# Kernel tuning notes

Hardware: AMD Instinct MI355X
Metric: run time of the kernel (lower is better)

## Reference

```python
import jax, jax.numpy as jnp
import numpy as np

B, N, F_IN = 8, 1024, 25   # batch, num_edges (GAT nodes), features_per_link = 1 + 8*num_bands
H, D = 8, 16               # num_heads, output_dim per head (hidden_size // num_heads)
NEG_INF = -9e15            # matches torch -9000000000000000.0


def setup_inputs() -> dict:
    key = jax.random.key(0)
    k1, k2, k3, k4 = jax.random.split(key, 4)
    node_feats = jax.random.normal(k1, (B, N, F_IN), dtype=jnp.float32)
    adj = jax.random.randint(k2, (B, N, N), 0, 2, dtype=jnp.int32)
    # Xavier-uniform-ish params per GATLayer.reset_parameters (gain for relu)
    gain = float(np.sqrt(2.0))
    limW = gain * np.sqrt(6.0 / (F_IN + D))
    lima = gain * np.sqrt(6.0 / (2 * D + 1))
    W = jax.random.uniform(k3, (H, F_IN, D), jnp.float32, -limW, limW)
    a = jax.random.uniform(k4, (H, 2 * D, 1), jnp.float32, -lima, lima)
    return {"node_feats": node_feats, "adj": adj, "W": W, "a": a}


def reference(node_feats, adj, W, a):
    d = W.shape[-1]
    # Wh: [B, H, N, D]
    Wh = jnp.einsum('bnf,hfd->bhnd', node_feats, W)
    # Additive attention: e_ij = <Wh_i, a_src> + <Wh_j, a_dst>  (no LeakyReLU in this module)
    a_src = a[:, :d, 0]   # [H, D]
    a_dst = a[:, d:, 0]   # [H, D]
    ei = jnp.einsum('bhnd,hd->bhn', Wh, a_src)  # [B, H, N]
    ej = jnp.einsum('bhnd,hd->bhn', Wh, a_dst)  # [B, H, N]
    e = ei[:, :, :, None] + ej[:, :, None, :]   # [B, H, N, N]
    mask = adj[:, None, :, :].astype(bool)      # [B, 1->H, N, N]
    e = jnp.where(mask, e, jnp.asarray(NEG_INF, e.dtype))
    alpha = jax.nn.softmax(e, axis=-1)          # dropout is identity at eval
    h_prime = jnp.einsum('bhij,bhjd->bhid', alpha, Wh)        # [B, H, N, D]
    h_prime = h_prime.transpose(0, 2, 1, 3).reshape(node_feats.shape[0], node_feats.shape[1], -1)
    return jax.nn.relu(h_prime), alpha
```

## Files before the change

### kernel.cpp

```cpp
#include <hip/hip_runtime.h>

#define L2E 1.44269504f

typedef short short8_t  __attribute__((ext_vector_type(8)));
typedef float fltx4     __attribute__((ext_vector_type(4)));
typedef int   intx4     __attribute__((ext_vector_type(4)));
typedef unsigned short ushort4_t __attribute__((ext_vector_type(4)));
typedef unsigned int uint32;

__device__ __forceinline__ unsigned short f2bf(float f) {
    uint32 u = __float_as_uint(f);
    u += 0x7FFFu + ((u >> 16) & 1u);
    return (unsigned short)(u >> 16);
}

__global__ __launch_bounds__(256) void prep_once(
    const float* __restrict__ x,
    const float* __restrict__ W,
    const float* __restrict__ a,
    float* __restrict__ pexp_ws,
    unsigned short* __restrict__ whb)
{
    int t  = blockIdx.x * 256 + threadIdx.x;
    int bh = t >> 10, n = t & 1023;
    int b  = bh >> 3, h = bh & 7;

    const float* xr = x + ((size_t)(b * 1024 + n)) * 25;
    const float* Wp = W + h * 400;
    const float* ap = a + h * 32;

    float xf[25];
    #pragma unroll
    for (int f = 0; f < 25; ++f) xf[f] = xr[f];

    int base = ((bh * 32 + (n >> 5)) * 64 + ((n >> 3) & 3) * 16) * 8 + (n & 7);
    float vj = 0.f;
    #pragma unroll
    for (int d = 0; d < 16; ++d) {
        float s = 0.f;
        #pragma unroll
        for (int f = 0; f < 25; ++f) s += xf[f] * Wp[f * 16 + d];
        vj += s * ap[16 + d];
        whb[base + d * 8] = f2bf(s);
    }
    pexp_ws[t] = exp2f(vj * L2E);
}

__global__ __launch_bounds__(256) void gat_main(
    const int*   __restrict__ adj,
    const float* __restrict__ pexp_ws,
    const unsigned short* __restrict__ whb,
    float* __restrict__ out0,
    float* __restrict__ out1)
{
    __shared__ __align__(16) unsigned short palds[16 * 1024];

    const int blk   = blockIdx.x;
    const int x8    = blk & 7;
    const int h     = (blk >> 3) & 7;
    const int s     = blk >> 6;
    const int c     = s * 8 + x8;
    const int b     = c >> 6;
    const int chunk = c & 63;
    const int bh    = b * 8 + h;
    const int wave  = threadIdx.x >> 6;
    const int lane  = threadIdx.x & 63;
    const int i0    = chunk * 16;

    const fltx4* pe4 = (const fltx4*)(pexp_ws + bh * 1024);
    fltx4 expr_[4];
    #pragma unroll
    for (int j0 = 0; j0 < 4; ++j0) expr_[j0] = pe4[j0 * 64 + lane];

    float* abase = out1 + (size_t)bh * 1024 * 1024;
    char*  ldsb  = (char*)palds;

    const intx4* adjb = (const intx4*)(adj + ((size_t)b * 1024 + i0 + wave * 4) * 1024);
    uint32 msk[4];
    #pragma unroll
    for (int r = 0; r < 4; ++r) {
        uint32 m = 0;
        #pragma unroll
        for (int j0 = 0; j0 < 4; ++j0) {
            intx4 a4 = adjb[r * 256 + j0 * 64 + lane];
            m |= (a4.x ? (1u << (j0 * 4 + 0)) : 0u);
            m |= (a4.y ? (1u << (j0 * 4 + 1)) : 0u);
            m |= (a4.z ? (1u << (j0 * 4 + 2)) : 0u);
            m |= (a4.w ? (1u << (j0 * 4 + 3)) : 0u);
        }
        msk[r] = m;
    }

    float sum[4];
    #pragma unroll
    for (int r = 0; r < 4; ++r) {
        float s0 = 0.f;
        const uint32 m = msk[r];
        #pragma unroll
        for (int j0 = 0; j0 < 4; ++j0) {
            fltx4 ev = expr_[j0];
            s0 += ((m >> (j0 * 4 + 0)) & 1u) ? ev.x : 0.f;
            s0 += ((m >> (j0 * 4 + 1)) & 1u) ? ev.y : 0.f;
            s0 += ((m >> (j0 * 4 + 2)) & 1u) ? ev.z : 0.f;
            s0 += ((m >> (j0 * 4 + 3)) & 1u) ? ev.w : 0.f;
        }
        sum[r] = s0;
    }

    #pragma unroll
    for (int off = 32; off; off >>= 1) {
        #pragma unroll
        for (int r = 0; r < 4; ++r) sum[r] += __shfl_xor(sum[r], off);
    }

    #pragma unroll
    for (int r = 0; r < 4; ++r) {
        const int rl = wave * 4 + r;
        const int i  = i0 + rl;
        const uint32 m = msk[r];
        const bool ok = sum[r] > 0.f;
        const float rinv = ok ? __builtin_amdgcn_rcpf(sum[r]) : 0.f;
        const float fb   = ok ? 0.f : (1.0f / 1024.0f);

        float* arow = abase + (size_t)i * 1024;
        const int swz  = (rl & 7) << 4;
        char* lrow = ldsb + rl * 2048;
        #pragma unroll
        for (int j0 = 0; j0 < 4; ++j0) {
            fltx4 ev = expr_[j0];
            fltx4 st;
            st.x = ((m >> (j0 * 4 + 0)) & 1u) ? ev.x * rinv + fb : fb;
            st.y = ((m >> (j0 * 4 + 1)) & 1u) ? ev.y * rinv + fb : fb;
            st.z = ((m >> (j0 * 4 + 2)) & 1u) ? ev.z * rinv + fb : fb;
            st.w = ((m >> (j0 * 4 + 3)) & 1u) ? ev.w * rinv + fb : fb;
            *(fltx4*)(arow + (j0 * 64 + lane) * 4) = st;
            ushort4_t bv;
            bv.x = f2bf(st.x); bv.y = f2bf(st.y);
            bv.z = f2bf(st.z); bv.w = f2bf(st.w);
            *(ushort4_t*)(lrow + (((j0 * 512) + lane * 8) ^ swz)) = bv;
        }
    }

    __syncthreads();

    if (wave == 0) {
        const int mrow = lane & 15;
        const int quad = lane >> 4;
        const int swz  = (mrow & 7) << 4;
        char* lrow = ldsb + mrow * 2048;
        const unsigned short* bbase = whb + (size_t)bh * 16384;

        fltx4 acc = {0.f, 0.f, 0.f, 0.f};
        #pragma unroll 4
        for (int ks = 0; ks < 32; ++ks) {
            short8_t afr = *(const short8_t*)(lrow + ((ks * 64 + quad * 16) ^ swz));
            short8_t bfr = *(const short8_t*)(bbase + ((ks * 64 + lane) << 3));
            acc = __builtin_amdgcn_mfma_f32_16x16x32_bf16(afr, bfr, acc, 0, 0, 0);
        }

        #pragma unroll
        for (int r = 0; r < 4; ++r) {
            int i = i0 + quad * 4 + r;
            float v = acc[r] > 0.f ? acc[r] : 0.f;
            out0[((size_t)(b * 1024 + i)) * 128 + h * 16 + mrow] = v;
        }
    }
}

__global__ __launch_bounds__(256) void gat_fused(
    const float* __restrict__ x, const int* __restrict__ adj,
    const float* __restrict__ W, const float* __restrict__ a,
    float* __restrict__ out0, float* __restrict__ out1)
{
    __shared__ __align__(16) unsigned short whb[32 * 64 * 8];
    __shared__ __align__(16) float ej_lds[1024];
    __shared__ float ei_lds[64];
    __shared__ float wa[64];

    const int bh    = blockIdx.x >> 4;
    const int chunk = blockIdx.x & 15;
    const int b     = bh >> 3;
    const int h     = bh & 7;
    const int tid   = threadIdx.x;
    const int wave  = tid >> 6;
    const int lane  = tid & 63;
    const int mrow  = lane & 15;
    const int quad  = lane >> 4;

    const float* Wp = W + h * 400;
    const float* ap = a + h * 32;
    const float* xb = x + (size_t)b * 1024 * 25;

    if (tid < 50) {
        int f = tid % 25, which = tid / 25;
        float s = 0.f;
        #pragma unroll
        for (int d = 0; d < 16; ++d) s += Wp[f * 16 + d] * ap[which * 16 + d];
        wa[which * 32 + f] = s;
    }
    __syncthreads();

    for (int s = 0; s < 4; ++s) {
        int n = tid + (s << 8);
        const float* xr = xb + n * 25;
        float xf[25];
        #pragma unroll
        for (int f = 0; f < 25; ++f) xf[f] = xr[f];
        float vi = 0.f, vj = 0.f;
        #pragma unroll
        for (int f = 0; f < 25; ++f) { vi += xf[f] * wa[f]; vj += xf[f] * wa[32 + f]; }
        ej_lds[n] = vj;
        if ((n >> 6) == chunk) ei_lds[n & 63] = vi;
        int base = (((n >> 5) * 64 + ((n >> 3) & 3) * 16) << 3) + (n & 7);
        #pragma unroll
        for (int d = 0; d < 16; ++d) {
            float s2 = 0.f;
            #pragma unroll
            for (int f = 0; f < 25; ++f) s2 += xf[f] * Wp[f * 16 + d];
            whb[base + d * 8] = f2bf(s2);
        }
    }
    __syncthreads();

    const int i0 = chunk * 64 + wave * 16;
    float* abase = out1 + (size_t)bh * 1024 * 1024;
    const fltx4* ej4 = (const fltx4*)ej_lds;

    for (int r = 0; r < 16; ++r) {
        int i = i0 + r;
        float s_ei = ei_lds[wave * 16 + r];
        const intx4* adj4 = (const intx4*)(adj + ((size_t)b * 1024 + i) * 1024);
        float p[16];
        float sum = 0.f;
        #pragma unroll
        for (int j0 = 0; j0 < 4; ++j0) {
            intx4 av = adj4[j0 * 64 + lane];
            fltx4 ev = ej4[j0 * 64 + lane];
            float p0 = av.x ? exp2f((s_ei + ev.x) * L2E) : 0.f;
            float p1 = av.y ? exp2f((s_ei + ev.y) * L2E) : 0.f;
            float p2 = av.z ? exp2f((s_ei + ev.z) * L2E) : 0.f;
            float p3 = av.w ? exp2f((s_ei + ev.w) * L2E) : 0.f;
            p[j0 * 4 + 0] = p0; p[j0 * 4 + 1] = p1;
            p[j0 * 4 + 2] = p2; p[j0 * 4 + 3] = p3;
            sum += (p0 + p1) + (p2 + p3);
        }
        #pragma unroll
        for (int off = 32; off; off >>= 1) sum += __shfl_xor(sum, off);
        float rinv;
        if (sum > 0.f) {
            rinv = __builtin_amdgcn_rcpf(sum);
        } else {
            rinv = 1.0f;
            #pragma unroll
            for (int k = 0; k < 16; ++k) p[k] = 1.0f / 1024.0f;
        }
        float* arow = abase + (size_t)i * 1024;
        #pragma unroll
        for (int j0 = 0; j0 < 4; ++j0) {
            fltx4 st;
            st.x = p[j0 * 4 + 0] * rinv; st.y = p[j0 * 4 + 1] * rinv;
            st.z = p[j0 * 4 + 2] * rinv; st.w = p[j0 * 4 + 3] * rinv;
            *(fltx4*)(arow + (j0 * 64 + lane) * 4) = st;
        }
    }

    __builtin_amdgcn_fence(__ATOMIC_ACQ_REL, "workgroup");

    const float* aptr = abase + (size_t)(i0 + mrow) * 1024 + quad * 8;
    fltx4 acc = {0.f, 0.f, 0.f, 0.f};
    for (int ks = 0; ks < 32; ++ks) {
        fltx4 a0 = *(const fltx4*)(aptr + ks * 32);
        fltx4 a1 = *(const fltx4*)(aptr + ks * 32 + 4);
        short8_t afr;
        #pragma unroll
        for (int q = 0; q < 4; ++q) {
            afr[q]     = (short)f2bf(a0[q]);
            afr[4 + q] = (short)f2bf(a1[q]);
        }
        short8_t bfr = *(const short8_t*)&whb[((ks * 64 + lane) << 3)];
        acc = __builtin_amdgcn_mfma_f32_16x16x32_bf16(afr, bfr, acc, 0, 0, 0);
    }
    #pragma unroll
    for (int r = 0; r < 4; ++r) {
        int i = i0 + quad * 4 + r;
        float v = acc[r] > 0.f ? acc[r] : 0.f;
        out0[((size_t)(b * 1024 + i)) * 128 + h * 16 + mrow] = v;
    }
}

extern "C" void kernel_launch(void* const* d_in, const int* in_sizes, int n_in,
                              void* d_out, int out_size, void* d_ws, size_t ws_size,
                              hipStream_t stream) {
    const float* x   = (const float*)d_in[0];
    const int*   adj = (const int*)d_in[1];
    const float* W   = (const float*)d_in[2];
    const float* a   = (const float*)d_in[3];

    float* out0 = (float*)d_out;
    float* out1 = out0 + (size_t)8 * 1024 * 128;

    const size_t WHB_BYTES = (size_t)64 * 16384 * 2;
    const size_t EJ_BYTES  = (size_t)64 * 1024 * 4;
    const size_t NEED      = WHB_BYTES + EJ_BYTES;

    if (ws_size >= NEED) {
        unsigned short* whb = (unsigned short*)d_ws;
        float* pexp_ws = (float*)((char*)d_ws + WHB_BYTES);
        prep_once<<<256, 256, 0, stream>>>(x, W, a, pexp_ws, whb);
        gat_main<<<4096, 256, 0, stream>>>(adj, pexp_ws, whb, out0, out1);
    } else {
        gat_fused<<<1024, 256, 0, stream>>>(x, adj, W, a, out0, out1);
    }
}
```

Before: 330.4 us.

## Give each wave its own 16-row tile with per-wave MFMA, drop block barrier

Each wave now handles 16 query rows instead of 4, so every wave runs its own bf16 MFMA accumulation from a private LDS tile. The block-wide __syncthreads and the wave-0-only matmul go away, and the grid shrinks from 4096 to 1024 blocks. Alpha rows are written with nontemporal stores, interleaved column block by column block with the MFMA k-steps. This removes the idle waves during the matmul and the barrier stall. In exchange each thread holds 16 mask and sum registers, which may lower occupancy, and there is less block-level parallelism.

```diff
diff --git a/kernel.cpp b/kernel.cpp
--- a/kernel.cpp
+++ b/kernel.cpp
@@ -53,19 +53,19 @@
     float* __restrict__ out0,
     float* __restrict__ out1)
 {
-    __shared__ __align__(16) unsigned short palds[16 * 1024];
+    __shared__ __align__(16) unsigned short tlds[4][16][256];
 
     const int blk   = blockIdx.x;
     const int x8    = blk & 7;
     const int h     = (blk >> 3) & 7;
     const int s     = blk >> 6;
     const int c     = s * 8 + x8;
-    const int b     = c >> 6;
-    const int chunk = c & 63;
+    const int b     = c >> 4;
+    const int chunk = c & 15;
     const int bh    = b * 8 + h;
     const int wave  = threadIdx.x >> 6;
     const int lane  = threadIdx.x & 63;
-    const int i0    = chunk * 16;
+    const int i0    = chunk * 64 + wave * 16;
 
     const fltx4* pe4 = (const fltx4*)(pexp_ws + bh * 1024);
     fltx4 expr_[4];
@@ -73,12 +73,11 @@
     for (int j0 = 0; j0 < 4; ++j0) expr_[j0] = pe4[j0 * 64 + lane];
 
     float* abase = out1 + (size_t)bh * 1024 * 1024;
-    char*  ldsb  = (char*)palds;
-
-    const intx4* adjb = (const intx4*)(adj + ((size_t)b * 1024 + i0 + wave * 4) * 1024);
-    uint32 msk[4];
-    #pragma unroll
-    for (int r = 0; r < 4; ++r) {
+
+    const intx4* adjb = (const intx4*)(adj + ((size_t)b * 1024 + i0) * 1024);
+    uint32 msk[16];
+    #pragma unroll
+    for (int r = 0; r < 16; ++r) {
         uint32 m = 0;
         #pragma unroll
         for (int j0 = 0; j0 < 4; ++j0) {
@@ -91,9 +90,9 @@
         msk[r] = m;
     }
 
-    float sum[4];
-    #pragma unroll
-    for (int r = 0; r < 4; ++r) {
+    float sum[16];
+    #pragma unroll
+    for (int r = 0; r < 16; ++r) {
         float s0 = 0.f;
         const uint32 m = msk[r];
         #pragma unroll
@@ -106,64 +105,53 @@
         }
         sum[r] = s0;
     }
-
     #pragma unroll
     for (int off = 32; off; off >>= 1) {
         #pragma unroll
-        for (int r = 0; r < 4; ++r) sum[r] += __shfl_xor(sum[r], off);
-    }
-
-    #pragma unroll
-    for (int r = 0; r < 4; ++r) {
-        const int rl = wave * 4 + r;
-        const int i  = i0 + rl;
-        const uint32 m = msk[r];
-        const bool ok = sum[r] > 0.f;
-        const float rinv = ok ? __builtin_amdgcn_rcpf(sum[r]) : 0.f;
-        const float fb   = ok ? 0.f : (1.0f / 1024.0f);
-
-        float* arow = abase + (size_t)i * 1024;
-        const int swz  = (rl & 7) << 4;
-        char* lrow = ldsb + rl * 2048;
-        #pragma unroll
-        for (int j0 = 0; j0 < 4; ++j0) {
-            fltx4 ev = expr_[j0];
+        for (int r = 0; r < 16; ++r) sum[r] += __shfl_xor(sum[r], off);
+    }
+
+    char* tl = (char*)&tlds[wave][0][0];
+    const unsigned short* bbase = whb + (size_t)bh * 16384;
+    const int mrow = lane & 15;
+    const int quad = lane >> 4;
+    fltx4 acc = {0.f, 0.f, 0.f, 0.f};
+
+    #pragma unroll
+    for (int j0 = 0; j0 < 4; ++j0) {
+        fltx4 ev = expr_[j0];
+        #pragma unroll
+        for (int r = 0; r < 16; ++r) {
+            const bool ok = sum[r] > 0.f;
+            const float rinv = ok ? __builtin_amdgcn_rcpf(sum[r]) : 0.f;
+            const float fbv  = ok ? 0.f : (1.0f / 1024.0f);
+            const uint32 m = msk[r] >> (j0 * 4);
             fltx4 st;
-            st.x = ((m >> (j0 * 4 + 0)) & 1u) ? ev.x * rinv + fb : fb;
-            st.y = ((m >> (j0 * 4 + 1)) & 1u) ? ev.y * rinv + fb : fb;
-            st.z = ((m >> (j0 * 4 + 2)) & 1u) ? ev.z * rinv + fb : fb;
-            st.w = ((m >> (j0 * 4 + 3)) & 1u) ? ev.w * rinv + fb : fb;
-            *(fltx4*)(arow + (j0 * 64 + lane) * 4) = st;
+            st.x = (m & 1u) ? ev.x * rinv + fbv : fbv;
+            st.y = (m & 2u) ? ev.y * rinv + fbv : fbv;
+            st.z = (m & 4u) ? ev.z * rinv + fbv : fbv;
+            st.w = (m & 8u) ? ev.w * rinv + fbv : fbv;
+            __builtin_nontemporal_store(st,
+                (fltx4*)(abase + (size_t)(i0 + r) * 1024 + j0 * 256 + lane * 4));
             ushort4_t bv;
             bv.x = f2bf(st.x); bv.y = f2bf(st.y);
             bv.z = f2bf(st.z); bv.w = f2bf(st.w);
-            *(ushort4_t*)(lrow + (((j0 * 512) + lane * 8) ^ swz)) = bv;
-        }
-    }
-
-    __syncthreads();
-
-    if (wave == 0) {
-        const int mrow = lane & 15;
-        const int quad = lane >> 4;
-        const int swz  = (mrow & 7) << 4;
-        char* lrow = ldsb + mrow * 2048;
-        const unsigned short* bbase = whb + (size_t)bh * 16384;
-
-        fltx4 acc = {0.f, 0.f, 0.f, 0.f};
-        #pragma unroll 4
-        for (int ks = 0; ks < 32; ++ks) {
-            short8_t afr = *(const short8_t*)(lrow + ((ks * 64 + quad * 16) ^ swz));
-            short8_t bfr = *(const short8_t*)(bbase + ((ks * 64 + lane) << 3));
+            *(ushort4_t*)(tl + r * 512 + ((lane * 8) ^ ((r & 7) << 4))) = bv;
+        }
+        #pragma unroll
+        for (int kl = 0; kl < 8; ++kl) {
+            short8_t afr = *(const short8_t*)(tl + mrow * 512 +
+                             ((kl * 64 + quad * 16) ^ ((mrow & 7) << 4)));
+            short8_t bfr = *(const short8_t*)(bbase + (((j0 * 8 + kl) * 64 + lane) << 3));
             acc = __builtin_amdgcn_mfma_f32_16x16x32_bf16(afr, bfr, acc, 0, 0, 0);
         }
-
-        #pragma unroll
-        for (int r = 0; r < 4; ++r) {
-            int i = i0 + quad * 4 + r;
-            float v = acc[r] > 0.f ? acc[r] : 0.f;
-            out0[((size_t)(b * 1024 + i)) * 128 + h * 16 + mrow] = v;
-        }
+    }
+
+    #pragma unroll
+    for (int r = 0; r < 4; ++r) {
+        const int i = i0 + quad * 4 + r;
+        float v = acc[r] > 0.f ? acc[r] : 0.f;
+        out0[((size_t)(b * 1024 + i)) * 128 + h * 16 + mrow] = v;
     }
 }
 
@@ -307,7 +295,7 @@
         unsigned short* whb = (unsigned short*)d_ws;
         float* pexp_ws = (float*)((char*)d_ws + WHB_BYTES);
         prep_once<<<256, 256, 0, stream>>>(x, W, a, pexp_ws, whb);
-        gat_main<<<4096, 256, 0, stream>>>(adj, pexp_ws, whb, out0, out1);
+        gat_main<<<1024, 256, 0, stream>>>(adj, pexp_ws, whb, out0, out1);
     } else {
         gat_fused<<<1024, 256, 0, stream>>>(x, adj, W, a, out0, out1);
     }
```

After: 366.7 us. 1.11x slower.

## Loop heads inside each block to reuse adjacency mask and give every wave MFMA work

Applied to the files above, without the earlier changes.

Each block now handles all 8 heads for a 16-row chunk, so the adjacency mask is loaded and packed once instead of once per head, and the grid shrinks from 4096 to 512 blocks. Each wave writes its own 4 rows into a private LDS tile and runs its own MFMA with only rows 0-3 meaningful, which removes the block-wide barrier and the single-wave GEMM tail. The alpha output now uses nontemporal stores. The cost is that three quarters of each MFMA's rows are wasted, and there are fewer, longer-running blocks to hide memory latency.

```diff
diff --git a/kernel.cpp b/kernel.cpp
--- a/kernel.cpp
+++ b/kernel.cpp
@@ -53,29 +53,18 @@
     float* __restrict__ out0,
     float* __restrict__ out1)
 {
-    __shared__ __align__(16) unsigned short palds[16 * 1024];
+    __shared__ __align__(16) unsigned short tlds[4][4][1024];
 
     const int blk   = blockIdx.x;
-    const int x8    = blk & 7;
-    const int h     = (blk >> 3) & 7;
-    const int s     = blk >> 6;
-    const int c     = s * 8 + x8;
-    const int b     = c >> 6;
-    const int chunk = c & 63;
-    const int bh    = b * 8 + h;
+    const int b     = blk >> 6;
+    const int chunk = blk & 63;
     const int wave  = threadIdx.x >> 6;
     const int lane  = threadIdx.x & 63;
-    const int i0    = chunk * 16;
-
-    const fltx4* pe4 = (const fltx4*)(pexp_ws + bh * 1024);
-    fltx4 expr_[4];
-    #pragma unroll
-    for (int j0 = 0; j0 < 4; ++j0) expr_[j0] = pe4[j0 * 64 + lane];
-
-    float* abase = out1 + (size_t)bh * 1024 * 1024;
-    char*  ldsb  = (char*)palds;
-
-    const intx4* adjb = (const intx4*)(adj + ((size_t)b * 1024 + i0 + wave * 4) * 1024);
+    const int i0    = chunk * 16 + wave * 4;
+    const int mrow  = lane & 15;
+    const int quad  = lane >> 4;
+
+    const intx4* adjb = (const intx4*)(adj + ((size_t)b * 1024 + i0) * 1024);
     uint32 msk[4];
     #pragma unroll
     for (int r = 0; r < 4; ++r) {
@@ -91,78 +80,77 @@
         msk[r] = m;
     }
 
-    float sum[4];
-    #pragma unroll
-    for (int r = 0; r < 4; ++r) {
-        float s0 = 0.f;
-        const uint32 m = msk[r];
-        #pragma unroll
-        for (int j0 = 0; j0 < 4; ++j0) {
-            fltx4 ev = expr_[j0];
-            s0 += ((m >> (j0 * 4 + 0)) & 1u) ? ev.x : 0.f;
-            s0 += ((m >> (j0 * 4 + 1)) & 1u) ? ev.y : 0.f;
-            s0 += ((m >> (j0 * 4 + 2)) & 1u) ? ev.z : 0.f;
-            s0 += ((m >> (j0 * 4 + 3)) & 1u) ? ev.w : 0.f;
-        }
-        sum[r] = s0;
-    }
-
-    #pragma unroll
-    for (int off = 32; off; off >>= 1) {
-        #pragma unroll
-        for (int r = 0; r < 4; ++r) sum[r] += __shfl_xor(sum[r], off);
-    }
-
-    #pragma unroll
-    for (int r = 0; r < 4; ++r) {
-        const int rl = wave * 4 + r;
-        const int i  = i0 + rl;
-        const uint32 m = msk[r];
-        const bool ok = sum[r] > 0.f;
-        const float rinv = ok ? __builtin_amdgcn_rcpf(sum[r]) : 0.f;
-        const float fb   = ok ? 0.f : (1.0f / 1024.0f);
-
-        float* arow = abase + (size_t)i * 1024;
-        const int swz  = (rl & 7) << 4;
-        char* lrow = ldsb + rl * 2048;
-        #pragma unroll
-        for (int j0 = 0; j0 < 4; ++j0) {
-            fltx4 ev = expr_[j0];
-            fltx4 st;
-            st.x = ((m >> (j0 * 4 + 0)) & 1u) ? ev.x * rinv + fb : fb;
-            st.y = ((m >> (j0 * 4 + 1)) & 1u) ? ev.y * rinv + fb : fb;
-            st.z = ((m >> (j0 * 4 + 2)) & 1u) ? ev.z * rinv + fb : fb;
-            st.w = ((m >> (j0 * 4 + 3)) & 1u) ? ev.w * rinv + fb : fb;
-            *(fltx4*)(arow + (j0 * 64 + lane) * 4) = st;
-            ushort4_t bv;
-            bv.x = f2bf(st.x); bv.y = f2bf(st.y);
-            bv.z = f2bf(st.z); bv.w = f2bf(st.w);
-            *(ushort4_t*)(lrow + (((j0 * 512) + lane * 8) ^ swz)) = bv;
-        }
-    }
-
-    __syncthreads();
-
-    if (wave == 0) {
-        const int mrow = lane & 15;
-        const int quad = lane >> 4;
-        const int swz  = (mrow & 7) << 4;
-        char* lrow = ldsb + mrow * 2048;
+    char* tl = (char*)&tlds[wave][0][0];
+
+    for (int h = 0; h < 8; ++h) {
+        const int bh = b * 8 + h;
+
+        const fltx4* pe4 = (const fltx4*)(pexp_ws + bh * 1024);
+        fltx4 ev[4];
+        #pragma unroll
+        for (int j0 = 0; j0 < 4; ++j0) ev[j0] = pe4[j0 * 64 + lane];
+
+        float sum[4];
+        #pragma unroll
+        for (int r = 0; r < 4; ++r) {
+            float s0 = 0.f;
+            const uint32 m = msk[r];
+            #pragma unroll
+            for (int j0 = 0; j0 < 4; ++j0) {
+                s0 += ((m >> (j0 * 4 + 0)) & 1u) ? ev[j0].x : 0.f;
+                s0 += ((m >> (j0 * 4 + 1)) & 1u) ? ev[j0].y : 0.f;
+                s0 += ((m >> (j0 * 4 + 2)) & 1u) ? ev[j0].z : 0.f;
+                s0 += ((m >> (j0 * 4 + 3)) & 1u) ? ev[j0].w : 0.f;
+            }
+            sum[r] = s0;
+        }
+        #pragma unroll
+        for (int off = 32; off; off >>= 1) {
+            #pragma unroll
+            for (int r = 0; r < 4; ++r) sum[r] += __shfl_xor(sum[r], off);
+        }
+
+        float* abase = out1 + (size_t)bh * 1024 * 1024;
+        #pragma unroll
+        for (int r = 0; r < 4; ++r) {
+            const bool ok = sum[r] > 0.f;
+            const float rinv = ok ? __builtin_amdgcn_rcpf(sum[r]) : 0.f;
+            const float fbv  = ok ? 0.f : (1.0f / 1024.0f);
+            const uint32 m = msk[r];
+            const int swz = r << 6;
+            #pragma unroll
+            for (int j0 = 0; j0 < 4; ++j0) {
+                fltx4 st;
+                st.x = ((m >> (j0 * 4 + 0)) & 1u) ? ev[j0].x * rinv + fbv : fbv;
+                st.y = ((m >> (j0 * 4 + 1)) & 1u) ? ev[j0].y * rinv + fbv : fbv;
+                st.z = ((m >> (j0 * 4 + 2)) & 1u) ? ev[j0].z * rinv + fbv : fbv;
+                st.w = ((m >> (j0 * 4 + 3)) & 1u) ? ev[j0].w * rinv + fbv : fbv;
+                __builtin_nontemporal_store(st,
+                    (fltx4*)(abase + (size_t)(i0 + r) * 1024 + j0 * 256 + lane * 4));
+                ushort4_t bv;
+                bv.x = f2bf(st.x); bv.y = f2bf(st.y);
+                bv.z = f2bf(st.z); bv.w = f2bf(st.w);
+                *(ushort4_t*)(tl + r * 2048 + ((j0 * 512 + lane * 8) ^ swz)) = bv;
+            }
+        }
+
         const unsigned short* bbase = whb + (size_t)bh * 16384;
-
+        const int arow = mrow & 3;
+        const int aswz = arow << 6;
         fltx4 acc = {0.f, 0.f, 0.f, 0.f};
-        #pragma unroll 4
+        #pragma unroll 8
         for (int ks = 0; ks < 32; ++ks) {
-            short8_t afr = *(const short8_t*)(lrow + ((ks * 64 + quad * 16) ^ swz));
+            short8_t afr = *(const short8_t*)(tl + arow * 2048 +
+                             ((ks * 64 + quad * 16) ^ aswz));
             short8_t bfr = *(const short8_t*)(bbase + ((ks * 64 + lane) << 3));
             acc = __builtin_amdgcn_mfma_f32_16x16x32_bf16(afr, bfr, acc, 0, 0, 0);
         }
-
-        #pragma unroll
-        for (int r = 0; r < 4; ++r) {
-            int i = i0 + quad * 4 + r;
-            float v = acc[r] > 0.f ? acc[r] : 0.f;
-            out0[((size_t)(b * 1024 + i)) * 128 + h * 16 + mrow] = v;
+        if (quad == 0) {
+            #pragma unroll
+            for (int r = 0; r < 4; ++r) {
+                float v = acc[r] > 0.f ? acc[r] : 0.f;
+                out0[((size_t)(b * 1024 + i0 + r)) * 128 + h * 16 + mrow] = v;
+            }
         }
     }
 }
@@ -307,7 +295,7 @@
         unsigned short* whb = (unsigned short*)d_ws;
         float* pexp_ws = (float*)((char*)d_ws + WHB_BYTES);
         prep_once<<<256, 256, 0, stream>>>(x, W, a, pexp_ws, whb);
-        gat_main<<<4096, 256, 0, stream>>>(adj, pexp_ws, whb, out0, out1);
+        gat_main<<<512, 256, 0, stream>>>(adj, pexp_ws, whb, out0, out1);
     } else {
         gat_fused<<<1024, 256, 0, stream>>>(x, adj, W, a, out0, out1);
     }
```

Result: faster. 302.5 us (-8.5%).
